# Performance work log

Measured on AMD Instinct MI355X. Metric: run time of the kernel, lower is better.

## Reference

```python
import jax, jax.numpy as jnp
import numpy as np

N, E, G, H = 50000, 800000, 64, 4
IN_DIM, HID, OUT = 768, 256, 128
EPS = 1e-5
SLOPE = 0.2


def _glorot(k, shape):
    lim = np.sqrt(6.0 / (shape[0] + shape[1])).astype(np.float32)
    return jax.random.uniform(k, shape, jnp.float32, -lim, lim)


def setup_inputs() -> dict:
    key = jax.random.key(0)
    ks = jax.random.split(key, 24)
    inp = {
        'x': jax.random.normal(ks[0], (N, IN_DIM), jnp.float32),
        'edge_index': jax.random.randint(ks[1], (2, E), 0, N, jnp.int32),
        'batch': jnp.sort(jax.random.randint(ks[2], (N,), 0, G, jnp.int32)),
    }
    dims = [(IN_DIM, HID), (HID, HID), (HID, OUT)]
    for i, (di, do) in enumerate(dims, start=1):
        c = do // H
        inp[f'W{i}'] = _glorot(ks[3 * i], (di, do))
        inp[f'asrc{i}'] = _glorot(ks[3 * i + 1], (H, c))
        inp[f'adst{i}'] = _glorot(ks[3 * i + 2], (H, c))
        inp[f'b{i}'] = jnp.zeros((do,), jnp.float32)
        inp[f'g{i}'] = jnp.ones((do,), jnp.float32)
        inp[f'be{i}'] = jnp.zeros((do,), jnp.float32)
    return inp


def gat_conv(x, src, dst, W, asrc, adst, b):
    # PyG GATConv, concat=True, negative_slope=0.2, self-loops pre-appended.
    n = x.shape[0]
    HC = W.shape[1]
    C = HC // H
    h = (x @ W).reshape(n, H, C)                 # [N,H,C]
    e_src = (h * asrc).sum(-1)                   # [N,H]
    e_dst = (h * adst).sum(-1)                   # [N,H]
    e = jax.nn.leaky_relu(e_src[src] + e_dst[dst], SLOPE)  # [E',H]
    m = jax.ops.segment_max(e, dst, num_segments=n)
    p = jnp.exp(e - m[dst])
    denom = jax.ops.segment_sum(p, dst, num_segments=n)
    alpha = p / denom[dst]                       # segment softmax over in-edges
    out = jax.ops.segment_sum(alpha[:, :, None] * h[src], dst, num_segments=n)
    return out.reshape(n, HC) + b


def layer_norm(x, g, b):
    mu = x.mean(-1, keepdims=True)
    var = x.var(-1, keepdims=True)
    return g * (x - mu) * jax.lax.rsqrt(var + EPS) + b


def reference(x, edge_index, batch, W1, asrc1, adst1, b1, g1, be1,
              W2, asrc2, adst2, b2, g2, be2, W3, asrc3, adst3, b3, g3, be3):
    n = x.shape[0]
    loops = jnp.arange(n, dtype=edge_index.dtype)
    src = jnp.concatenate([edge_index[0], loops])
    dst = jnp.concatenate([edge_index[1], loops])
    h = gat_conv(x, src, dst, W1, asrc1, adst1, b1)
    h = layer_norm(jax.nn.elu(h), g1, be1)
    h = gat_conv(h, src, dst, W2, asrc2, adst2, b2)
    h = layer_norm(jax.nn.elu(h), g2, be2)
    h = gat_conv(h, src, dst, W3, asrc3, adst3, b3)
    node_emb = layer_norm(h, g3, be3)
    s = jax.ops.segment_sum(node_emb, batch, num_segments=G)
    cnt = jax.ops.segment_sum(jnp.ones((n, 1), node_emb.dtype), batch, num_segments=G)
    graph_emb = s / jnp.maximum(cnt, 1.0)
    return (node_emb, graph_emb)
```

## Files before the change

kernel.cpp:

```cpp
#include <hip/hip_runtime.h>
#include <math.h>

__device__ __forceinline__ float lrelu(float v) { return v > 0.f ? v : 0.2f * v; }
__device__ __forceinline__ float bf2f(ushort u) {
    return __uint_as_float(((unsigned int)u) << 16);
}
__device__ __forceinline__ ushort f2bf(float f) {
    unsigned int x = __float_as_uint(f);
    return (ushort)((x + 0x7fffu + ((x >> 16) & 1u)) >> 16);
}
__device__ __forceinline__ float wave_allred_sum(float v) {
#pragma unroll
    for (int off = 1; off < 64; off <<= 1) v += __shfl_xor(v, off, 64);
    return v;
}

typedef short bf16x8 __attribute__((ext_vector_type(8)));
typedef float f32x4 __attribute__((ext_vector_type(4)));
typedef ushort u16x8 __attribute__((ext_vector_type(8)));
typedef ushort u16x4 __attribute__((ext_vector_type(4)));

typedef const __attribute__((address_space(1))) void* gas_ptr;
typedef __attribute__((address_space(3))) void* las_ptr;
__device__ __forceinline__ void gload_lds16(const void* g, void* l) {
    __builtin_amdgcn_global_load_lds((gas_ptr)g, (las_ptr)l, 16, 0, 0);
}

__global__ void hist_kernel(const int* __restrict__ dstrow, int* __restrict__ cnt,
                            int Etot, int E) {
    int i = blockIdx.x * blockDim.x + threadIdx.x;
    if (i >= Etot) return;
    int d = (i < E) ? dstrow[i] : (i - E);
    atomicAdd(&cnt[d], 1);
}

__global__ __launch_bounds__(256) void scan1_kernel(const int* __restrict__ cnt,
                                                    int* __restrict__ out,
                                                    int* __restrict__ btot, int n) {
    __shared__ int s[256];
    int i = blockIdx.x * 256 + threadIdx.x;
    int v = (i < n) ? cnt[i] : 0;
    s[threadIdx.x] = v;
    __syncthreads();
    for (int off = 1; off < 256; off <<= 1) {
        int t = (threadIdx.x >= off) ? s[threadIdx.x - off] : 0;
        __syncthreads();
        s[threadIdx.x] += t;
        __syncthreads();
    }
    if (i < n) out[i] = s[threadIdx.x];
    if (threadIdx.x == 255) btot[blockIdx.x] = s[255];
}
__global__ __launch_bounds__(1024) void scan2_kernel(int* __restrict__ btot, int nb) {
    __shared__ int s[1024];
    int tid = threadIdx.x;
    int v = (tid < nb) ? btot[tid] : 0;
    s[tid] = v;
    __syncthreads();
    for (int off = 1; off < 1024; off <<= 1) {
        int t = (tid >= off) ? s[tid - off] : 0;
        __syncthreads();
        s[tid] += t;
        __syncthreads();
    }
    if (tid < nb) btot[tid] = s[tid] - v;
}
__global__ void scan3_kernel(const int* __restrict__ scanned, const int* __restrict__ btot,
                             int* __restrict__ rowptr, int n) {
    int i = blockIdx.x * 256 + threadIdx.x;
    if (i < n) rowptr[i + 1] = scanned[i] + btot[i >> 8];
    if (i == 0) rowptr[0] = 0;
}

__global__ void fill_kernel(const int* __restrict__ srcrow, const int* __restrict__ dstrow,
                            const int* __restrict__ rowptr, int* __restrict__ pos,
                            int* __restrict__ srcs, int Etot, int E) {
    int i = blockIdx.x * blockDim.x + threadIdx.x;
    if (i >= Etot) return;
    int d = (i < E) ? dstrow[i] : (i - E);
    int s = (i < E) ? srcrow[i] : (i - E);
    int p = atomicAdd(&pos[d], 1);
    srcs[rowptr[d] + p] = s;
}

__global__ __launch_bounds__(256) void wconv_kernel(const float* __restrict__ W,
                                                    ushort* __restrict__ Wt, int K, int N) {
    __shared__ float t[32][33];
    int k0 = blockIdx.x * 32, n0 = blockIdx.y * 32;
    int tx = threadIdx.x & 31, ty = threadIdx.x >> 5;
#pragma unroll
    for (int i = 0; i < 32; i += 8)
        t[ty + i][tx] = W[(size_t)(k0 + ty + i) * N + n0 + tx];
    __syncthreads();
#pragma unroll
    for (int i = 0; i < 32; i += 8)
        Wt[(size_t)(n0 + ty + i) * K + k0 + tx] = f2bf(t[tx][ty + i]);
}

template <typename TA>
__global__ __launch_bounds__(256) void gemm_mfma2(const TA* __restrict__ A,
                                                  const ushort* __restrict__ Wt,
                                                  ushort* __restrict__ C,
                                                  int M, int K, int N) {
    constexpr bool F32A = (sizeof(TA) == 4);
    constexpr int ASZ = F32A ? 16384 : 8192;
    __shared__ __align__(16) unsigned char smem[2 * ASZ + 16384];

    int tid = threadIdx.x;
    int wv = tid >> 6, lane = tid & 63;
    int quad = lane >> 4, mrow = lane & 15;

    int nwg = gridDim.x * gridDim.y;
    int id = blockIdx.y * gridDim.x + blockIdx.x;
    int q8 = nwg >> 3, r8 = nwg & 7;
    int xcd = id & 7, loc = id >> 3;
    int wgid = (xcd < r8 ? xcd * (q8 + 1) : r8 * (q8 + 1) + (xcd - r8) * q8) + loc;
    int n0 = (wgid % gridDim.x) * 128;
    int m0 = (wgid / gridDim.x) * 128;

    f32x4 acc[2][8] = {};

    auto stageA = [&](int kt, int buf) {
        unsigned char* lb = smem + buf * ASZ;
        if constexpr (F32A) {
#pragma unroll
            for (int q = 0; q < 4; q++) {
                int row = q * 32 + (tid >> 3);
                int gch = (tid & 7) ^ (row & 7);
                int rc = min(m0 + row, M - 1);
                gload_lds16((const float*)A + (size_t)rc * K + kt + gch * 4,
                            lb + q * 4096 + tid * 16);
            }
        } else {
#pragma unroll
            for (int q = 0; q < 2; q++) {
                int row = q * 64 + (tid >> 2);
                int gch = (tid & 3) ^ ((row & 3) ^ ((row >> 2) & 1));
                int rc = min(m0 + row, M - 1);
                gload_lds16((const ushort*)A + (size_t)rc * K + kt + gch * 8,
                            lb + q * 4096 + tid * 16);
            }
        }
    };
    auto stageB = [&](int kt, int buf) {
        unsigned char* lb = smem + 2 * ASZ + buf * 8192;
#pragma unroll
        for (int q = 0; q < 2; q++) {
            int row = q * 64 + (tid >> 2);
            int gch = (tid & 3) ^ ((row & 3) ^ ((row >> 2) & 1));
            gload_lds16(Wt + (size_t)(n0 + row) * K + kt + gch * 8,
                        lb + q * 4096 + tid * 16);
        }
    };

    int nsteps = K >> 5;
    stageA(0, 0);
    stageB(0, 0);
    __syncthreads();

    for (int s = 0; s < nsteps; s++) {
        int kt = s << 5;
        if (s + 1 < nsteps) {
            stageA(kt + 32, (s + 1) & 1);
            stageB(kt + 32, (s + 1) & 1);
        }
        const unsigned char* la = smem + (s & 1) * ASZ;
        const unsigned char* lbB = smem + 2 * ASZ + (s & 1) * 8192;

        bf16x8 afrag[2], bfrag[8];
#pragma unroll
        for (int r = 0; r < 2; r++) {
            int row = wv * 32 + r * 16 + mrow;
            if constexpr (F32A) {
                int f = row & 7;
                float4 x0 = *(const float4*)(la + row * 128 + ((quad * 2 + 0) ^ f) * 16);
                float4 x1 = *(const float4*)(la + row * 128 + ((quad * 2 + 1) ^ f) * 16);
                union { bf16x8 v; ushort u[8]; } t;
                t.u[0] = f2bf(x0.x); t.u[1] = f2bf(x0.y);
                t.u[2] = f2bf(x0.z); t.u[3] = f2bf(x0.w);
                t.u[4] = f2bf(x1.x); t.u[5] = f2bf(x1.y);
                t.u[6] = f2bf(x1.z); t.u[7] = f2bf(x1.w);
                afrag[r] = t.v;
            } else {
                int f = (row & 3) ^ ((row >> 2) & 1);
                afrag[r] = *(const bf16x8*)(la + row * 64 + (quad ^ f) * 16);
            }
        }
#pragma unroll
        for (int c = 0; c < 8; c++) {
            int row = c * 16 + mrow;
            int f = (row & 3) ^ ((row >> 2) & 1);
            bfrag[c] = *(const bf16x8*)(lbB + row * 64 + (quad ^ f) * 16);
        }
#pragma unroll
        for (int r = 0; r < 2; r++)
#pragma unroll
            for (int c = 0; c < 8; c++)
                acc[r][c] = __builtin_amdgcn_mfma_f32_16x16x32_bf16(afrag[r], bfrag[c],
                                                                    acc[r][c], 0, 0, 0);
        __syncthreads();
    }

    int col = lane & 15;
#pragma unroll
    for (int r = 0; r < 2; r++) {
#pragma unroll
        for (int c = 0; c < 8; c++) {
#pragma unroll
            for (int reg = 0; reg < 4; reg++) {
                int gm = m0 + wv * 32 + r * 16 + quad * 4 + reg;
                int gn = n0 + c * 16 + col;
                if (gm < M) C[(size_t)gm * N + gn] = f2bf(acc[r][c][reg]);
            }
        }
    }
}

template <int VPL>
__global__ __launch_bounds__(256) void attn_wave(const ushort* __restrict__ H,
                                                 const float* __restrict__ asrc,
                                                 const float* __restrict__ adst,
                                                 float* __restrict__ es, float* __restrict__ ed,
                                                 int N) {
    constexpr int HC = VPL * 64;
    int lane = threadIdx.x & 63;
    int node = (blockIdx.x * blockDim.x + threadIdx.x) >> 6;
    if (node >= N) return;
    const ushort* hp = H + (size_t)node * HC + lane * VPL;
    float esum = 0.f, dsum = 0.f;
#pragma unroll
    for (int j = 0; j < VPL; j++) {
        float h = bf2f(hp[j]);
        int ch = lane * VPL + j;
        esum += h * asrc[ch];
        dsum += h * adst[ch];
    }
#pragma unroll
    for (int off = 1; off < 16; off <<= 1) {
        esum += __shfl_xor(esum, off, 64);
        dsum += __shfl_xor(dsum, off, 64);
    }
    if ((lane & 15) == 0) {
        int hh = lane >> 4;
        es[node * 4 + hh] = esum;
        ed[node * 4 + hh] = dsum;
    }
}

template <int HC>
__global__ __launch_bounds__(256) void agg_gather(
    const ushort* __restrict__ H, const float* __restrict__ es, const float* __restrict__ ed,
    const int* __restrict__ rowptr, const int* __restrict__ srcs,
    const float* __restrict__ bias, const float* __restrict__ gamma,
    const float* __restrict__ beta, ushort* __restrict__ XoutB, float* __restrict__ XoutF,
    int N, int applyElu) {
    constexpr int EPL = HC / 32;
    int lane = threadIdx.x & 63;
    int node = (blockIdx.x * blockDim.x + threadIdx.x) >> 6;
    if (node >= N) return;
    int base = rowptr[node];
    int deg = rowptr[node + 1] - base;
    float4 ed4 = *(const float4*)&ed[node * 4];

    float4 sm = make_float4(0.f, 0.f, 0.f, 0.f);
    for (int i = lane; i < deg; i += 64) {
        int s = srcs[base + i];
        float4 e4 = *(const float4*)&es[(size_t)s * 4];
        sm.x += __expf(lrelu(e4.x + ed4.x));
        sm.y += __expf(lrelu(e4.y + ed4.y));
        sm.z += __expf(lrelu(e4.z + ed4.z));
        sm.w += __expf(lrelu(e4.w + ed4.w));
    }
    sm.x = wave_allred_sum(sm.x); sm.y = wave_allred_sum(sm.y);
    sm.z = wave_allred_sum(sm.z); sm.w = wave_allred_sum(sm.w);

    int half = lane >> 5;
    int ln = lane & 31;
    int hh = ln >> 3;
    float rd_h = 1.f / ((hh == 0) ? sm.x : (hh == 1) ? sm.y : (hh == 2) ? sm.z : sm.w);
    float edh = (hh == 0) ? ed4.x : (hh == 1) ? ed4.y : (hh == 2) ? ed4.z : ed4.w;

    float acc[EPL];
#pragma unroll
    for (int j = 0; j < EPL; j++) acc[j] = 0.f;
    const ushort* Hl = H + ln * EPL;

    int i = half;
    for (; i + 2 < deg; i += 4) {
        int s0 = srcs[base + i];
        int s1 = srcs[base + i + 2];
        float e0 = es[(size_t)s0 * 4 + hh];
        float e1 = es[(size_t)s1 * 4 + hh];
        const ushort* hp0 = Hl + (size_t)s0 * HC;
        const ushort* hp1 = Hl + (size_t)s1 * HC;
        float a0 = __expf(lrelu(e0 + edh)) * rd_h;
        float a1 = __expf(lrelu(e1 + edh)) * rd_h;
        if constexpr (EPL == 8) {
            u16x8 h0 = *(const u16x8*)hp0;
            u16x8 h1 = *(const u16x8*)hp1;
#pragma unroll
            for (int j = 0; j < 8; j++)
                acc[j] += a0 * bf2f(h0[j]) + a1 * bf2f(h1[j]);
        } else {
            u16x4 h0 = *(const u16x4*)hp0;
            u16x4 h1 = *(const u16x4*)hp1;
#pragma unroll
            for (int j = 0; j < 4; j++)
                acc[j] += a0 * bf2f(h0[j]) + a1 * bf2f(h1[j]);
        }
    }
    if (i < deg) {
        int s = srcs[base + i];
        float a = __expf(lrelu(es[(size_t)s * 4 + hh] + edh)) * rd_h;
        const ushort* hp = Hl + (size_t)s * HC;
        if constexpr (EPL == 8) {
            u16x8 hv = *(const u16x8*)hp;
#pragma unroll
            for (int j = 0; j < 8; j++) acc[j] += a * bf2f(hv[j]);
        } else {
            u16x4 hv = *(const u16x4*)hp;
#pragma unroll
            for (int j = 0; j < 4; j++) acc[j] += a * bf2f(hv[j]);
        }
    }

#pragma unroll
    for (int j = 0; j < EPL; j++) acc[j] += __shfl_xor(acc[j], 32, 64);

    float v[EPL];
    float s1 = 0.f, s2 = 0.f;
#pragma unroll
    for (int j = 0; j < EPL; j++) {
        int ch = ln * EPL + j;
        float t = acc[j] + bias[ch];
        if (applyElu) t = (t > 0.f) ? t : (__expf(t) - 1.f);
        v[j] = t;
        s1 += t;
        s2 += t * t;
    }
    s1 = wave_allred_sum(s1);
    s2 = wave_allred_sum(s2);
    float mu = s1 / (2.f * HC);
    float var = s2 / (2.f * HC) - mu * mu;
    float rs = rsqrtf(var + 1e-5f);
    if (half == 0) {
#pragma unroll
        for (int j = 0; j < EPL; j++) {
            int ch = ln * EPL + j;
            float o = gamma[ch] * (v[j] - mu) * rs + beta[ch];
            if (XoutF) XoutF[(size_t)node * HC + ch] = o;
            else XoutB[(size_t)node * HC + ch] = f2bf(o);
        }
    }
}

__global__ __launch_bounds__(128) void gsum_kernel(const float* __restrict__ node_emb,
                                                   const int* __restrict__ batch,
                                                   float* __restrict__ gsum,
                                                   int* __restrict__ gcnt, int N) {
    int start = blockIdx.x * 256;
    if (start >= N) return;
    int end = min(start + 256, N);
    int ch = threadIdx.x;
    float acc = 0.f;
    int runlen = 0;
    int curg = batch[start];
    for (int n = start; n < end; n++) {
        int g = batch[n];
        if (g != curg) {
            atomicAdd(&gsum[curg * 128 + ch], acc);
            if (ch == 0) atomicAdd(&gcnt[curg], runlen);
            acc = 0.f; runlen = 0; curg = g;
        }
        acc += node_emb[(size_t)n * 128 + ch];
        runlen++;
    }
    atomicAdd(&gsum[curg * 128 + ch], acc);
    if (ch == 0) atomicAdd(&gcnt[curg], runlen);
}

__global__ void gfinal_kernel(const float* __restrict__ gsum, const int* __restrict__ gcnt,
                              float* __restrict__ out, int Gn) {
    int i = blockIdx.x * blockDim.x + threadIdx.x;
    if (i >= Gn * 128) return;
    int g = i >> 7;
    out[i] = gsum[i] / fmaxf((float)gcnt[g], 1.f);
}

extern "C" void kernel_launch(void* const* d_in, const int* in_sizes, int n_in, void* d_out,
                              int out_size, void* d_ws, size_t ws_size, hipStream_t stream) {
    const float* x = (const float*)d_in[0];
    const int* ei = (const int*)d_in[1];
    const int* batch = (const int*)d_in[2];
    const float* W1 = (const float*)d_in[3];
    const float* as1 = (const float*)d_in[4];
    const float* ad1 = (const float*)d_in[5];
    const float* b1 = (const float*)d_in[6];
    const float* g1 = (const float*)d_in[7];
    const float* be1 = (const float*)d_in[8];
    const float* W2 = (const float*)d_in[9];
    const float* as2 = (const float*)d_in[10];
    const float* ad2 = (const float*)d_in[11];
    const float* b2 = (const float*)d_in[12];
    const float* g2 = (const float*)d_in[13];
    const float* be2 = (const float*)d_in[14];
    const float* W3 = (const float*)d_in[15];
    const float* as3 = (const float*)d_in[16];
    const float* ad3 = (const float*)d_in[17];
    const float* b3 = (const float*)d_in[18];
    const float* g3 = (const float*)d_in[19];
    const float* be3 = (const float*)d_in[20];

    int N = in_sizes[2];
    int E = in_sizes[1] / 2;
    int Etot = E + N;

    char* w = (char*)d_ws;
    size_t off = 0;
    auto alloc = [&](size_t bytes) -> void* {
        void* p = w + off;
        off += (bytes + 255) & ~(size_t)255;
        return p;
    };
    int* cnt = (int*)alloc((size_t)N * 4);
    int* pos = (int*)alloc((size_t)N * 4);
    float* gsum = (float*)alloc(64 * 128 * 4);
    int* gcnt = (int*)alloc(64 * 4);
    size_t zbytes = off;
    int* scantmp = (int*)alloc((size_t)N * 4);
    int* btot = (int*)alloc(1024 * 4);
    int* rowptr = (int*)alloc((size_t)(N + 1) * 4);
    int* srcs = (int*)alloc((size_t)Etot * 4);
    float* es = (float*)alloc((size_t)N * 16);
    float* ed = (float*)alloc((size_t)N * 16);
    ushort* Hb = (ushort*)alloc((size_t)N * 256 * 2);
    ushort* Xb = (ushort*)alloc((size_t)N * 256 * 2);
    ushort* wt1 = (ushort*)alloc((size_t)768 * 256 * 2);
    ushort* wt2 = (ushort*)alloc((size_t)256 * 256 * 2);
    ushort* wt3 = (ushort*)alloc((size_t)256 * 128 * 2);

    hipMemsetAsync(d_ws, 0, zbytes, stream);

    const int* srcrow = ei;
    const int* dstrow = ei + E;

    wconv_kernel<<<dim3(768 / 32, 256 / 32), 256, 0, stream>>>(W1, wt1, 768, 256);
    wconv_kernel<<<dim3(256 / 32, 256 / 32), 256, 0, stream>>>(W2, wt2, 256, 256);
    wconv_kernel<<<dim3(256 / 32, 128 / 32), 256, 0, stream>>>(W3, wt3, 256, 128);

    int eb = (Etot + 255) / 256;
    int nb = (N + 255) / 256;
    hist_kernel<<<eb, 256, 0, stream>>>(dstrow, cnt, Etot, E);
    scan1_kernel<<<nb, 256, 0, stream>>>(cnt, scantmp, btot, N);
    scan2_kernel<<<1, 1024, 0, stream>>>(btot, nb);
    scan3_kernel<<<nb, 256, 0, stream>>>(scantmp, btot, rowptr, N);
    fill_kernel<<<eb, 256, 0, stream>>>(srcrow, dstrow, rowptr, pos, srcs, Etot, E);

    int mT = (N + 127) / 128;
    int nodeWaveBlocks = (N + 3) / 4;

    float* out_node = (float*)d_out;
    float* out_graph = (float*)d_out + (size_t)N * 128;

    gemm_mfma2<float><<<dim3(2, mT), 256, 0, stream>>>(x, wt1, Hb, N, 768, 256);
    attn_wave<4><<<nodeWaveBlocks, 256, 0, stream>>>(Hb, as1, ad1, es, ed, N);
    agg_gather<256><<<nodeWaveBlocks, 256, 0, stream>>>(Hb, es, ed, rowptr, srcs, b1, g1, be1,
                                                        Xb, nullptr, N, 1);
    gemm_mfma2<ushort><<<dim3(2, mT), 256, 0, stream>>>(Xb, wt2, Hb, N, 256, 256);
    attn_wave<4><<<nodeWaveBlocks, 256, 0, stream>>>(Hb, as2, ad2, es, ed, N);
    agg_gather<256><<<nodeWaveBlocks, 256, 0, stream>>>(Hb, es, ed, rowptr, srcs, b2, g2, be2,
                                                        Xb, nullptr, N, 1);
    gemm_mfma2<ushort><<<dim3(1, mT), 256, 0, stream>>>(Xb, wt3, Hb, N, 256, 128);
    attn_wave<2><<<nodeWaveBlocks, 256, 0, stream>>>(Hb, as3, ad3, es, ed, N);
    agg_gather<128><<<nodeWaveBlocks, 256, 0, stream>>>(Hb, es, ed, rowptr, srcs, b3, g3, be3,
                                                        nullptr, out_node, N, 0);
    gsum_kernel<<<(N + 255) / 256, 128, 0, stream>>>(out_node, batch, gsum, gcnt, N);
    gfinal_kernel<<<(64 * 128 + 255) / 256, 256, 0, stream>>>(gsum, gcnt, out_graph, 64);
}
```

Before: 778.6 us.

## Process four nodes per wave in aggregation with 16-lane groups

The GAT aggregation kernel changes from one 64-lane wave per node (two half-waves splitting edges) to one 16-lane group per node, so each wave handles four nodes. Each lane now holds 16 or 8 channels and walks every edge itself, which removes the cross-half shuffle and the idle half on output writes. The aim is better lane utilisation for low-degree nodes (about 17 edges on average). In exchange each lane carries more registers and a longer serial edge loop, and load imbalance between the four nodes in a wave can appear.

```diff
diff --git a/kernel.cpp b/kernel.cpp
--- a/kernel.cpp
+++ b/kernel.cpp
@@ -18,7 +18,6 @@
 typedef short bf16x8 __attribute__((ext_vector_type(8)));
 typedef float f32x4 __attribute__((ext_vector_type(4)));
 typedef ushort u16x8 __attribute__((ext_vector_type(8)));
-typedef ushort u16x4 __attribute__((ext_vector_type(4)));
 
 typedef const __attribute__((address_space(1))) void* gas_ptr;
 typedef __attribute__((address_space(3))) void* las_ptr;
@@ -254,16 +253,16 @@
     const float* __restrict__ bias, const float* __restrict__ gamma,
     const float* __restrict__ beta, ushort* __restrict__ XoutB, float* __restrict__ XoutF,
     int N, int applyElu) {
-    constexpr int EPL = HC / 32;
-    int lane = threadIdx.x & 63;
-    int node = (blockIdx.x * blockDim.x + threadIdx.x) >> 6;
+    constexpr int EPL = HC / 16;
+    int ln = threadIdx.x & 15;
+    int node = (blockIdx.x * blockDim.x + threadIdx.x) >> 4;
     if (node >= N) return;
     int base = rowptr[node];
     int deg = rowptr[node + 1] - base;
     float4 ed4 = *(const float4*)&ed[node * 4];
 
     float4 sm = make_float4(0.f, 0.f, 0.f, 0.f);
-    for (int i = lane; i < deg; i += 64) {
+    for (int i = ln; i < deg; i += 16) {
         int s = srcs[base + i];
         float4 e4 = *(const float4*)&es[(size_t)s * 4];
         sm.x += __expf(lrelu(e4.x + ed4.x));
@@ -271,12 +270,15 @@
         sm.z += __expf(lrelu(e4.z + ed4.z));
         sm.w += __expf(lrelu(e4.w + ed4.w));
     }
-    sm.x = wave_allred_sum(sm.x); sm.y = wave_allred_sum(sm.y);
-    sm.z = wave_allred_sum(sm.z); sm.w = wave_allred_sum(sm.w);
-
-    int half = lane >> 5;
-    int ln = lane & 31;
-    int hh = ln >> 3;
+#pragma unroll
+    for (int off = 1; off < 16; off <<= 1) {
+        sm.x += __shfl_xor(sm.x, off, 64);
+        sm.y += __shfl_xor(sm.y, off, 64);
+        sm.z += __shfl_xor(sm.z, off, 64);
+        sm.w += __shfl_xor(sm.w, off, 64);
+    }
+
+    int hh = ln >> 2;
     float rd_h = 1.f / ((hh == 0) ? sm.x : (hh == 1) ? sm.y : (hh == 2) ? sm.z : sm.w);
     float edh = (hh == 0) ? ed4.x : (hh == 1) ? ed4.y : (hh == 2) ? ed4.z : ed4.w;
 
@@ -285,27 +287,31 @@
     for (int j = 0; j < EPL; j++) acc[j] = 0.f;
     const ushort* Hl = H + ln * EPL;
 
-    int i = half;
-    for (; i + 2 < deg; i += 4) {
+    int i = 0;
+    for (; i + 2 <= deg; i += 2) {
         int s0 = srcs[base + i];
-        int s1 = srcs[base + i + 2];
+        int s1 = srcs[base + i + 1];
         float e0 = es[(size_t)s0 * 4 + hh];
         float e1 = es[(size_t)s1 * 4 + hh];
         const ushort* hp0 = Hl + (size_t)s0 * HC;
         const ushort* hp1 = Hl + (size_t)s1 * HC;
         float a0 = __expf(lrelu(e0 + edh)) * rd_h;
         float a1 = __expf(lrelu(e1 + edh)) * rd_h;
-        if constexpr (EPL == 8) {
+        if constexpr (EPL == 16) {
+            u16x8 h0a = *(const u16x8*)hp0;
+            u16x8 h0b = *(const u16x8*)(hp0 + 8);
+            u16x8 h1a = *(const u16x8*)hp1;
+            u16x8 h1b = *(const u16x8*)(hp1 + 8);
+#pragma unroll
+            for (int j = 0; j < 8; j++) {
+                acc[j] += a0 * bf2f(h0a[j]) + a1 * bf2f(h1a[j]);
+                acc[j + 8] += a0 * bf2f(h0b[j]) + a1 * bf2f(h1b[j]);
+            }
+        } else {
             u16x8 h0 = *(const u16x8*)hp0;
             u16x8 h1 = *(const u16x8*)hp1;
 #pragma unroll
             for (int j = 0; j < 8; j++)
-                acc[j] += a0 * bf2f(h0[j]) + a1 * bf2f(h1[j]);
-        } else {
-            u16x4 h0 = *(const u16x4*)hp0;
-            u16x4 h1 = *(const u16x4*)hp1;
-#pragma unroll
-            for (int j = 0; j < 4; j++)
                 acc[j] += a0 * bf2f(h0[j]) + a1 * bf2f(h1[j]);
         }
     }
@@ -313,19 +319,20 @@
         int s = srcs[base + i];
         float a = __expf(lrelu(es[(size_t)s * 4 + hh] + edh)) * rd_h;
         const ushort* hp = Hl + (size_t)s * HC;
-        if constexpr (EPL == 8) {
+        if constexpr (EPL == 16) {
+            u16x8 ha = *(const u16x8*)hp;
+            u16x8 hb = *(const u16x8*)(hp + 8);
+#pragma unroll
+            for (int j = 0; j < 8; j++) {
+                acc[j] += a * bf2f(ha[j]);
+                acc[j + 8] += a * bf2f(hb[j]);
+            }
+        } else {
             u16x8 hv = *(const u16x8*)hp;
 #pragma unroll
             for (int j = 0; j < 8; j++) acc[j] += a * bf2f(hv[j]);
-        } else {
-            u16x4 hv = *(const u16x4*)hp;
-#pragma unroll
-            for (int j = 0; j < 4; j++) acc[j] += a * bf2f(hv[j]);
-        }
-    }
-
-#pragma unroll
-    for (int j = 0; j < EPL; j++) acc[j] += __shfl_xor(acc[j], 32, 64);
+        }
+    }
 
     float v[EPL];
     float s1 = 0.f, s2 = 0.f;
@@ -338,19 +345,20 @@
         s1 += t;
         s2 += t * t;
     }
-    s1 = wave_allred_sum(s1);
-    s2 = wave_allred_sum(s2);
-    float mu = s1 / (2.f * HC);
-    float var = s2 / (2.f * HC) - mu * mu;
+#pragma unroll
+    for (int off = 1; off < 16; off <<= 1) {
+        s1 += __shfl_xor(s1, off, 64);
+        s2 += __shfl_xor(s2, off, 64);
+    }
+    float mu = s1 / (float)HC;
+    float var = s2 / (float)HC - mu * mu;
     float rs = rsqrtf(var + 1e-5f);
-    if (half == 0) {
-#pragma unroll
-        for (int j = 0; j < EPL; j++) {
-            int ch = ln * EPL + j;
-            float o = gamma[ch] * (v[j] - mu) * rs + beta[ch];
-            if (XoutF) XoutF[(size_t)node * HC + ch] = o;
-            else XoutB[(size_t)node * HC + ch] = f2bf(o);
-        }
+#pragma unroll
+    for (int j = 0; j < EPL; j++) {
+        int ch = ln * EPL + j;
+        float o = gamma[ch] * (v[j] - mu) * rs + beta[ch];
+        if (XoutF) XoutF[(size_t)node * HC + ch] = o;
+        else XoutB[(size_t)node * HC + ch] = f2bf(o);
     }
 }
 
@@ -458,22 +466,23 @@
 
     int mT = (N + 127) / 128;
     int nodeWaveBlocks = (N + 3) / 4;
+    int nodeGroupBlocks = (N + 15) / 16;
 
     float* out_node = (float*)d_out;
     float* out_graph = (float*)d_out + (size_t)N * 128;
 
     gemm_mfma2<float><<<dim3(2, mT), 256, 0, stream>>>(x, wt1, Hb, N, 768, 256);
     attn_wave<4><<<nodeWaveBlocks, 256, 0, stream>>>(Hb, as1, ad1, es, ed, N);
-    agg_gather<256><<<nodeWaveBlocks, 256, 0, stream>>>(Hb, es, ed, rowptr, srcs, b1, g1, be1,
-                                                        Xb, nullptr, N, 1);
+    agg_gather<256><<<nodeGroupBlocks, 256, 0, stream>>>(Hb, es, ed, rowptr, srcs, b1, g1, be1,
+                                                         Xb, nullptr, N, 1);
     gemm_mfma2<ushort><<<dim3(2, mT), 256, 0, stream>>>(Xb, wt2, Hb, N, 256, 256);
     attn_wave<4><<<nodeWaveBlocks, 256, 0, stream>>>(Hb, as2, ad2, es, ed, N);
-    agg_gather<256><<<nodeWaveBlocks, 256, 0, stream>>>(Hb, es, ed, rowptr, srcs, b2, g2, be2,
-                                                        Xb, nullptr, N, 1);
+    agg_gather<256><<<nodeGroupBlocks, 256, 0, stream>>>(Hb, es, ed, rowptr, srcs, b2, g2, be2,
+                                                         Xb, nullptr, N, 1);
     gemm_mfma2<ushort><<<dim3(1, mT), 256, 0, stream>>>(Xb, wt3, Hb, N, 256, 128);
     attn_wave<2><<<nodeWaveBlocks, 256, 0, stream>>>(Hb, as3, ad3, es, ed, N);
-    agg_gather<128><<<nodeWaveBlocks, 256, 0, stream>>>(Hb, es, ed, rowptr, srcs, b3, g3, be3,
-                                                        nullptr, out_node, N, 0);
+    agg_gather<128><<<nodeGroupBlocks, 256, 0, stream>>>(Hb, es, ed, rowptr, srcs, b3, g3, be3,
+                                                         nullptr, out_node, N, 0);
     gsum_kernel<<<(N + 255) / 256, 128, 0, stream>>>(out_node, batch, gsum, gcnt, N);
     gfinal_kernel<<<(64 * 128 + 255) / 256, 256, 0, stream>>>(gsum, gcnt, out_graph, 64);
 }
```

After: 813.0 us. 4.4% more time.
